# Kernel tuning notes

Hardware: AMD Instinct MI355X
Metric: run time of the kernel (lower is better)

## Reference

```python
import jax, jax.numpy as jnp
import numpy as np

N_NODES = 100000
N_EDGES = 1600000
D_IN = 64
D_HID = 64
NEG_SLOPE = 0.01  # torch leaky_relu default


def _sage_conv(x, src, dst, W_l, b_l, W_r):
    # PyG SAGEConv (mean aggr): lin_l(mean_j x_j) + lin_r(x_i)
    n = x.shape[0]
    msg = x[src]  # [E, D] irregular gather
    agg = jax.ops.segment_sum(msg, dst, num_segments=n)
    deg = jax.ops.segment_sum(jnp.ones((src.shape[0],), x.dtype), dst, num_segments=n)
    mean = agg / jnp.maximum(deg, 1.0)[:, None]
    return mean @ W_l.T + b_l + x @ W_r.T


def setup_inputs() -> dict:
    key = jax.random.key(0)
    ks = jax.random.split(key, 12)
    x = jax.random.normal(ks[0], (N_NODES, D_IN), dtype=jnp.float32)
    edge_index = jax.random.randint(ks[1], (2, N_EDGES), 0, N_NODES, dtype=jnp.int64)
    s = 1.0 / np.sqrt(D_IN)
    params = {}
    dims = [(D_IN, D_HID), (D_HID, D_HID), (D_HID, D_HID)]
    ki = 2
    for i, (din, dout) in enumerate(dims, start=1):
        sc = 1.0 / np.sqrt(din)
        params[f'W_l{i}'] = jax.random.uniform(ks[ki], (dout, din), minval=-sc, maxval=sc, dtype=jnp.float32); ki += 1
        params[f'b_l{i}'] = jnp.zeros((dout,), jnp.float32)
        params[f'W_r{i}'] = jax.random.uniform(ks[ki], (dout, din), minval=-sc, maxval=sc, dtype=jnp.float32); ki += 1
    sc = 1.0 / np.sqrt(D_HID)
    params['W_out'] = jax.random.uniform(ks[ki], (1, D_HID), minval=-sc, maxval=sc, dtype=jnp.float32)
    params['b_out'] = jnp.zeros((1,), jnp.float32)
    return {'x': x, 'edge_index': edge_index, **params}


def reference(x, edge_index, W_l1, b_l1, W_r1, W_l2, b_l2, W_r2, W_l3, b_l3, W_r3, W_out, b_out):
    src, dst = edge_index[0], edge_index[1]
    h = x
    for (Wl, bl, Wr) in ((W_l1, b_l1, W_r1), (W_l2, b_l2, W_r2), (W_l3, b_l3, W_r3)):
        h = _sage_conv(h, src, dst, Wl, bl, Wr)
        h = jnp.where(h >= 0, h, NEG_SLOPE * h)
        # dropout is identity in eval mode
    return h @ W_out.T + b_out  # [N, 1]
```

## Files before the change

kernel.cpp:

```cpp
#include <hip/hip_runtime.h>
#include <hip/hip_fp16.h>

#define D 64
#define NEG_SLOPE 0.01f
#define CB_SHIFT 9
#define CB_NODES 512
#define MAXCB 256
#define CHUNK 4096
#define BCAP 10240
#define SADJ_CAP 10240
#define CGRID 256

typedef _Float16 f16x8 __attribute__((ext_vector_type(8)));
typedef float    f32x4 __attribute__((ext_vector_type(4)));

struct ScatSmem {
    int hist[MAXCB];
    int lofs[MAXCB];
    int gbase[MAXCB];
    int cur[MAXCB];
    int swsum[4];
    unsigned spk[CHUNK];
    unsigned char sbk[CHUNK];
};

__device__ __forceinline__ int detect64(const void* __restrict__ ei) {
    int lane = threadIdx.x & 63;
    int v = ((const int*)ei)[2 * lane + 1];
    return (__ballot(v != 0) == 0ULL) ? 1 : 0;
}

__device__ __forceinline__ int edge_at(const void* __restrict__ ei, long long idx, int is64) {
    if (is64) return (int)((const long long*)ei)[idx];
    return ((const int*)ei)[idx];
}

__device__ __forceinline__ void scatter_body(ScatSmem& sm,
        const void* __restrict__ ei, long long E,
        int* __restrict__ bcursor, unsigned* __restrict__ ebuf,
        int ncb, int bid) {
    int t = threadIdx.x;
    sm.hist[t] = 0;
    int is64 = detect64(ei);
    __syncthreads();
    long long start = (long long)bid * CHUNK;
    int ccnt = (int)min((long long)CHUNK, E - start);

    for (int i = t; i < ccnt; i += 256) {
        int d = edge_at(ei, E + start + i, is64);
        atomicAdd(&sm.hist[d >> CB_SHIFT], 1);
    }
    __syncthreads();
    {
        int v = sm.hist[t];
        int lane = t & 63, w = t >> 6;
        int inc = v;
        for (int off = 1; off < 64; off <<= 1) {
            int u = __shfl_up(inc, off, 64);
            if (lane >= off) inc += u;
        }
        if (lane == 63) sm.swsum[w] = inc;
        __syncthreads();
        int wof = 0;
        for (int i = 0; i < w; ++i) wof += sm.swsum[i];
        sm.lofs[t] = wof + inc - v;
    }
    if (t < ncb && sm.hist[t]) sm.gbase[t] = atomicAdd(&bcursor[t], sm.hist[t]);
    __syncthreads();
    sm.cur[t] = sm.lofs[t];
    __syncthreads();

    for (int i = t; i < ccnt; i += 256) {
        int s = edge_at(ei, start + i, is64);
        int d = edge_at(ei, E + start + i, is64);
        int b = d >> CB_SHIFT;
        int slot = atomicAdd(&sm.cur[b], 1);
        sm.spk[slot] = ((unsigned)s << CB_SHIFT) | (unsigned)(d & (CB_NODES - 1));
        sm.sbk[slot] = (unsigned char)b;
    }
    __syncthreads();

    for (int i = t; i < ccnt; i += 256) {
        int b = sm.sbk[i];
        int dst = sm.gbase[b] + (i - sm.lofs[b]);
        if (dst < BCAP) ebuf[(size_t)b * BCAP + dst] = sm.spk[i];
    }
}

__device__ __forceinline__ void conv_body(const float* __restrict__ x,
        _Float16* __restrict__ x16, long long U, int cid,
        const float* __restrict__ Wl1, const float* __restrict__ Wr1,
        const float* __restrict__ Wl2, const float* __restrict__ Wr2,
        const float* __restrict__ Wl3, const float* __restrict__ Wr3,
        _Float16* __restrict__ W16) {
    int t = threadIdx.x;
    for (long long u = (long long)cid * 256 + t; u < U; u += (long long)CGRID * 256) {
        const float* s = x + u * 8;
        const float4 v0 = *(const float4*)s;
        const float4 v1 = *(const float4*)(s + 4);
        f16x8 o = { (_Float16)v0.x, (_Float16)v0.y, (_Float16)v0.z, (_Float16)v0.w,
                    (_Float16)v1.x, (_Float16)v1.y, (_Float16)v1.z, (_Float16)v1.w };
        *(f16x8*)(x16 + u * 8) = o;
    }
    if (cid == 0) {
        const float* Ws[6] = { Wl1, Wr1, Wl2, Wr2, Wl3, Wr3 };
#pragma unroll
        for (int m = 0; m < 6; ++m) {
            const float* src = Ws[m];
            _Float16* dst = W16 + m * 4096;
            for (int i = t; i < 4096; i += 256) dst[i] = (_Float16)src[i];
        }
    }
}

__global__ __launch_bounds__(256, 6) void scatter_conv_kernel(
        const void* __restrict__ ei, long long E,
        int* __restrict__ bcursor, unsigned* __restrict__ ebuf, int ncb, int sgrid,
        const float* __restrict__ x, _Float16* __restrict__ x16, long long U,
        const float* __restrict__ Wl1, const float* __restrict__ Wr1,
        const float* __restrict__ Wl2, const float* __restrict__ Wr2,
        const float* __restrict__ Wl3, const float* __restrict__ Wr3,
        _Float16* __restrict__ W16) {
    __shared__ ScatSmem sm;
    if ((int)blockIdx.x < sgrid)
        scatter_body(sm, ei, E, bcursor, ebuf, ncb, blockIdx.x);
    else
        conv_body(x, x16, U, blockIdx.x - sgrid, Wl1, Wr1, Wl2, Wr2, Wl3, Wr3, W16);
}

__global__ __launch_bounds__(256) void sage_gemm_kernel(
        const _Float16* __restrict__ Hin, const _Float16* __restrict__ MH,
        const _Float16* __restrict__ W16,
        const float* __restrict__ bl,
        _Float16* __restrict__ Hout,
        const float* __restrict__ Wout, const float* __restrict__ bout,
        float* __restrict__ out, int N, int final_flag) {
    int t = threadIdx.x, w = t >> 6, lane = t & 63;
    int lr = lane & 15;
    int lk = lane >> 4;
    int rbase = (int)blockIdx.x * 128 + w * 32;

    f16x8 ah[2][2], am[2][2];
#pragma unroll
    for (int mt = 0; mt < 2; ++mt) {
        int gn = rbase + mt * 16 + lr;
        if (gn >= N) gn = N - 1;
        const _Float16* hp = Hin + (size_t)gn * D + lk * 8;
        const _Float16* mp = MH  + (size_t)gn * D + lk * 8;
        ah[mt][0] = *(const f16x8*)hp;  ah[mt][1] = *(const f16x8*)(hp + 32);
        am[mt][0] = *(const f16x8*)mp;  am[mt][1] = *(const f16x8*)(mp + 32);
    }

    f32x4 acc[2][4];
#pragma unroll
    for (int mt = 0; mt < 2; ++mt)
#pragma unroll
        for (int nt = 0; nt < 4; ++nt)
            acc[mt][nt] = (f32x4){0.f, 0.f, 0.f, 0.f};

    const _Float16* Wl = W16;
    const _Float16* Wr = W16 + 4096;
#pragma unroll
    for (int nt = 0; nt < 4; ++nt) {
        const _Float16* pl = Wl + (nt * 16 + lr) * D + lk * 8;
        const _Float16* pr = Wr + (nt * 16 + lr) * D + lk * 8;
        f16x8 b0 = *(const f16x8*)pl;  f16x8 b1 = *(const f16x8*)(pl + 32);
        f16x8 c0 = *(const f16x8*)pr;  f16x8 c1 = *(const f16x8*)(pr + 32);
        acc[0][nt] = __builtin_amdgcn_mfma_f32_16x16x32_f16(am[0][0], b0, acc[0][nt], 0, 0, 0);
        acc[0][nt] = __builtin_amdgcn_mfma_f32_16x16x32_f16(am[0][1], b1, acc[0][nt], 0, 0, 0);
        acc[0][nt] = __builtin_amdgcn_mfma_f32_16x16x32_f16(ah[0][0], c0, acc[0][nt], 0, 0, 0);
        acc[0][nt] = __builtin_amdgcn_mfma_f32_16x16x32_f16(ah[0][1], c1, acc[0][nt], 0, 0, 0);
        acc[1][nt] = __builtin_amdgcn_mfma_f32_16x16x32_f16(am[1][0], b0, acc[1][nt], 0, 0, 0);
        acc[1][nt] = __builtin_amdgcn_mfma_f32_16x16x32_f16(am[1][1], b1, acc[1][nt], 0, 0, 0);
        acc[1][nt] = __builtin_amdgcn_mfma_f32_16x16x32_f16(ah[1][0], c0, acc[1][nt], 0, 0, 0);
        acc[1][nt] = __builtin_amdgcn_mfma_f32_16x16x32_f16(ah[1][1], c1, acc[1][nt], 0, 0, 0);
    }

    float blv[4];
#pragma unroll
    for (int nt = 0; nt < 4; ++nt) blv[nt] = bl[nt * 16 + lr];

    if (!final_flag) {
#pragma unroll
        for (int mt = 0; mt < 2; ++mt)
#pragma unroll
            for (int r = 0; r < 4; ++r) {
                int gn = rbase + mt * 16 + lk * 4 + r;
                if (gn < N) {
#pragma unroll
                    for (int nt = 0; nt < 4; ++nt) {
                        float y = acc[mt][nt][r] + blv[nt];
                        y = (y >= 0.f) ? y : NEG_SLOPE * y;
                        Hout[(size_t)gn * D + nt * 16 + lr] = (_Float16)y;
                    }
                }
            }
    } else {
        float wv[4];
#pragma unroll
        for (int nt = 0; nt < 4; ++nt) wv[nt] = Wout[nt * 16 + lr];
        float bo = bout[0];
#pragma unroll
        for (int mt = 0; mt < 2; ++mt)
#pragma unroll
            for (int r = 0; r < 4; ++r) {
                float p = 0.f;
#pragma unroll
                for (int nt = 0; nt < 4; ++nt) {
                    float y = acc[mt][nt][r] + blv[nt];
                    y = (y >= 0.f) ? y : NEG_SLOPE * y;
                    p += y * wv[nt];
                }
                p += __shfl_xor(p, 1, 64);
                p += __shfl_xor(p, 2, 64);
                p += __shfl_xor(p, 4, 64);
                p += __shfl_xor(p, 8, 64);
                int gn = rbase + mt * 16 + lk * 4 + r;
                if (lr == 0 && gn < N) out[gn] = p + bo;
            }
    }
}

__global__ __launch_bounds__(256) void finefill_kernel(
        const unsigned* __restrict__ ebuf, const int* __restrict__ bcount,
        int* __restrict__ rowptr, int* __restrict__ adj, int N, int ncb) {
    __shared__ int cnt[CB_NODES];
    __shared__ int cur[CB_NODES];
    __shared__ int wpart[4];
    __shared__ int wsum4[4];
    __shared__ int se0;
    __shared__ int sAdj[SADJ_CAP];
    int t = threadIdx.x;
    int b = blockIdx.x;

    {
        int v = (t < ncb) ? min(bcount[t], BCAP) : 0;
        int lane = t & 63, w = t >> 6;
        int inc = v;
        for (int off = 1; off < 64; off <<= 1) {
            int u = __shfl_up(inc, off, 64);
            if (lane >= off) inc += u;
        }
        if (lane == 63) wsum4[w] = inc;
        __syncthreads();
        int wof = 0;
        for (int iw = 0; iw < w; ++iw) wof += wsum4[iw];
        int ex = wof + inc - v;
        if (t == b) se0 = ex;
        if (b == 0 && t == 0)
            rowptr[N] = wsum4[0] + wsum4[1] + wsum4[2] + wsum4[3];
    }
    __syncthreads();
    int e0 = se0;
    int len = min(bcount[b], BCAP);
    int nb = b << CB_SHIFT;
    const unsigned* slab = ebuf + (size_t)b * BCAP;

    cnt[2 * t] = 0; cnt[2 * t + 1] = 0;
    __syncthreads();
    for (int i = t; i < len; i += 256) {
        unsigned p = slab[i];
        atomicAdd(&cnt[p & (CB_NODES - 1)], 1);
    }
    __syncthreads();

    int c0 = cnt[2 * t], c1 = cnt[2 * t + 1];
    int s = c0 + c1;
    int lane = t & 63, wv = t >> 6;
    int inc = s;
    for (int off = 1; off < 64; off <<= 1) {
        int u = __shfl_up(inc, off, 64);
        if (lane >= off) inc += u;
    }
    if (lane == 63) wpart[wv] = inc;
    __syncthreads();
    int wof = 0;
    for (int w = 0; w < wv; ++w) wof += wpart[w];
    int ex = wof + inc - s;
    cur[2 * t] = ex; cur[2 * t + 1] = ex + c0;
    {
        int g = nb + 2 * t;
        if (g < N)     rowptr[g]     = e0 + ex;
        if (g + 1 < N) rowptr[g + 1] = e0 + ex + c0;
    }
    __syncthreads();

    int big = (len > SADJ_CAP);
    for (int i = t; i < len; i += 256) {
        unsigned p = slab[i];
        int dl = (int)(p & (CB_NODES - 1));
        int src = (int)(p >> CB_SHIFT);
        int pos = atomicAdd(&cur[dl], 1);
        if (big) adj[e0 + pos] = src;
        else     sAdj[pos] = src;
    }
    __syncthreads();
    if (!big) {
        for (int i = t; i < len; i += 256) adj[e0 + i] = sAdj[i];
    }
}

__global__ __launch_bounds__(256) void agg_kernel(
        const _Float16* __restrict__ H,
        const int* __restrict__ rowptr, const int* __restrict__ adj,
        _Float16* __restrict__ MH, int N) {
    int tid = blockIdx.x * blockDim.x + threadIdx.x;
    int i = tid >> 3;
    int sub = tid & 7;
    if (i >= N) return;

    int b0 = rowptr[i], b1 = rowptr[i + 1];
    float a0 = 0.f, a1 = 0.f, a2 = 0.f, a3 = 0.f;
    float a4 = 0.f, a5 = 0.f, a6 = 0.f, a7 = 0.f;
    size_t cofs = (size_t)(sub << 3);

    int e = b0;
    int nfull = (b1 - b0) >> 2;
#pragma unroll 2
    for (int q = 0; q < nfull; ++q) {
        int s0 = adj[e], s1 = adj[e + 1], s2 = adj[e + 2], s3 = adj[e + 3];
        e += 4;
        union { float4 f4; __half2 h2[4]; } u0, u1, u2, u3;
        u0.f4 = *(const float4*)(H + (size_t)s0 * D + cofs);
        u1.f4 = *(const float4*)(H + (size_t)s1 * D + cofs);
        u2.f4 = *(const float4*)(H + (size_t)s2 * D + cofs);
        u3.f4 = *(const float4*)(H + (size_t)s3 * D + cofs);
#define ACC8(u) { \
        float2 v0 = __half22float2(u.h2[0]); float2 v1 = __half22float2(u.h2[1]); \
        float2 v2 = __half22float2(u.h2[2]); float2 v3 = __half22float2(u.h2[3]); \
        a0 += v0.x; a1 += v0.y; a2 += v1.x; a3 += v1.y; \
        a4 += v2.x; a5 += v2.y; a6 += v3.x; a7 += v3.y; }
        ACC8(u0) ACC8(u1) ACC8(u2) ACC8(u3)
    }
    for (; e < b1; ++e) {
        int s = adj[e];
        union { float4 f4; __half2 h2[4]; } u;
        u.f4 = *(const float4*)(H + (size_t)s * D + cofs);
        ACC8(u)
    }
#undef ACC8

    float inv = 1.0f / fmaxf((float)(b1 - b0), 1.0f);
    f16x8 o = { (_Float16)(a0 * inv), (_Float16)(a1 * inv),
                (_Float16)(a2 * inv), (_Float16)(a3 * inv),
                (_Float16)(a4 * inv), (_Float16)(a5 * inv),
                (_Float16)(a6 * inv), (_Float16)(a7 * inv) };
    *(f16x8*)(MH + (size_t)i * D + cofs) = o;
}

extern "C" void kernel_launch(void* const* d_in, const int* in_sizes, int n_in,
                              void* d_out, int out_size, void* d_ws, size_t ws_size,
                              hipStream_t stream) {
    const float* x    = (const float*)d_in[0];
    const void*  ei   = d_in[1];
    const float* Wl1  = (const float*)d_in[2];
    const float* bl1  = (const float*)d_in[3];
    const float* Wr1  = (const float*)d_in[4];
    const float* Wl2  = (const float*)d_in[5];
    const float* bl2  = (const float*)d_in[6];
    const float* Wr2  = (const float*)d_in[7];
    const float* Wl3  = (const float*)d_in[8];
    const float* bl3  = (const float*)d_in[9];
    const float* Wr3  = (const float*)d_in[10];
    const float* Wout = (const float*)d_in[11];
    const float* bout = (const float*)d_in[12];
    float* out = (float*)d_out;

    int       N = in_sizes[0] / D;
    long long E = (long long)in_sizes[1] / 2;
    int ncb = (N + CB_NODES - 1) >> CB_SHIFT;
    long long U = (long long)N * D / 8;

    char* ws = (char*)d_ws;
    size_t off = 256;
    int* bcursor = (int*)(ws + off); off += 1024;
    int* rowptr = (int*)(ws + off); off += (((size_t)(N + 1) * 4 + 255) / 256) * 256;
    int* adj    = (int*)(ws + off); off += (((size_t)E * 4 + 255) / 256) * 256;
    unsigned* ebuf = (unsigned*)(ws + off); off += (size_t)ncb * BCAP * 4;
    _Float16* x16 = (_Float16*)(ws + off); off += (size_t)N * D * 2;
    _Float16* mh  = (_Float16*)(ws + off); off += (size_t)N * D * 2;
    _Float16* hA  = (_Float16*)(ws + off); off += (size_t)N * D * 2;
    _Float16* hB  = (_Float16*)(ws + off); off += (size_t)N * D * 2;
    _Float16* W16 = (_Float16*)(ws + off); off += 6 * 4096 * 2;

    int sgrid = (int)((E + CHUNK - 1) / CHUNK);
    int ggrid = (N + 127) / 128;
    int agrid = (N * 8 + 255) / 256;

    hipMemsetAsync(bcursor, 0, 1024, stream);

    scatter_conv_kernel<<<sgrid + CGRID, 256, 0, stream>>>(
        ei, E, bcursor, ebuf, ncb, sgrid,
        x, x16, U, Wl1, Wr1, Wl2, Wr2, Wl3, Wr3, W16);
    finefill_kernel<<<ncb, 256, 0, stream>>>(ebuf, bcursor, rowptr, adj, N, ncb);
    agg_kernel<<<agrid, 256, 0, stream>>>(x16, rowptr, adj, mh, N);
    sage_gemm_kernel<<<ggrid, 256, 0, stream>>>(x16, mh, W16, bl1, hA,
                                                Wout, bout, out, N, 0);
    agg_kernel<<<agrid, 256, 0, stream>>>(hA, rowptr, adj, mh, N);
    sage_gemm_kernel<<<ggrid, 256, 0, stream>>>(hA, mh, W16 + 2 * 4096, bl2, hB,
                                                Wout, bout, out, N, 0);
    agg_kernel<<<agrid, 256, 0, stream>>>(hB, rowptr, adj, mh, N);
    sage_gemm_kernel<<<ggrid, 256, 0, stream>>>(hB, mh, W16 + 4 * 4096, bl3, hA,
                                                Wout, bout, out, N, 1);
}
```

Before: 272.8 us.

## Fuse neighbor mean aggregation into SAGE GEMM kernel via shared memory

Each layer's aggregation kernel and GEMM kernel are merged into one kernel. Every block first gathers and averages neighbor features for its 128 nodes into padded shared memory, then runs the MFMA GEMM reading the mean from LDS. This removes the global round trip of the mean buffer and three kernel launches. In exchange, the gather now runs with fewer threads per node-group: 100k nodes over 782 blocks, with each thread looping over 4 nodes serially. That may reduce memory-level parallelism for the irregular gather.

```diff
diff --git a/kernel.cpp b/kernel.cpp
--- a/kernel.cpp
+++ b/kernel.cpp
@@ -10,6 +10,7 @@
 #define BCAP 10240
 #define SADJ_CAP 10240
 #define CGRID 256
+#define SAH 72
 
 typedef _Float16 f16x8 __attribute__((ext_vector_type(8)));
 typedef float    f32x4 __attribute__((ext_vector_type(4)));
@@ -128,17 +129,70 @@
         conv_body(x, x16, U, blockIdx.x - sgrid, Wl1, Wr1, Wl2, Wr2, Wl3, Wr3, W16);
 }
 
-__global__ __launch_bounds__(256) void sage_gemm_kernel(
-        const _Float16* __restrict__ Hin, const _Float16* __restrict__ MH,
+__global__ __launch_bounds__(256) void agg_gemm_kernel(
+        const _Float16* __restrict__ Hin,
+        const int* __restrict__ rowptr, const int* __restrict__ adj,
         const _Float16* __restrict__ W16,
         const float* __restrict__ bl,
         _Float16* __restrict__ Hout,
         const float* __restrict__ Wout, const float* __restrict__ bout,
         float* __restrict__ out, int N, int final_flag) {
-    int t = threadIdx.x, w = t >> 6, lane = t & 63;
+    __shared__ _Float16 smh[128 * SAH];
+    int t = threadIdx.x;
+    int node_base = (int)blockIdx.x * 128;
+
+    {
+        int g = t >> 3;
+        int sub = t & 7;
+        size_t cofs = (size_t)(sub << 3);
+#pragma unroll
+        for (int p = 0; p < 4; ++p) {
+            int local = p * 32 + g;
+            int i = node_base + local;
+            float a0 = 0.f, a1 = 0.f, a2 = 0.f, a3 = 0.f;
+            float a4 = 0.f, a5 = 0.f, a6 = 0.f, a7 = 0.f;
+            float inv = 0.f;
+            if (i < N) {
+                int b0 = rowptr[i], b1 = rowptr[i + 1];
+                int e = b0;
+                int nfull = (b1 - b0) >> 2;
+                for (int q = 0; q < nfull; ++q) {
+                    int s0 = adj[e], s1 = adj[e + 1], s2 = adj[e + 2], s3 = adj[e + 3];
+                    e += 4;
+                    union { float4 f4; __half2 h2[4]; } u0, u1, u2, u3;
+                    u0.f4 = *(const float4*)(Hin + (size_t)s0 * D + cofs);
+                    u1.f4 = *(const float4*)(Hin + (size_t)s1 * D + cofs);
+                    u2.f4 = *(const float4*)(Hin + (size_t)s2 * D + cofs);
+                    u3.f4 = *(const float4*)(Hin + (size_t)s3 * D + cofs);
+#define ACC8(u) { \
+        float2 v0 = __half22float2(u.h2[0]); float2 v1 = __half22float2(u.h2[1]); \
+        float2 v2 = __half22float2(u.h2[2]); float2 v3 = __half22float2(u.h2[3]); \
+        a0 += v0.x; a1 += v0.y; a2 += v1.x; a3 += v1.y; \
+        a4 += v2.x; a5 += v2.y; a6 += v3.x; a7 += v3.y; }
+                    ACC8(u0) ACC8(u1) ACC8(u2) ACC8(u3)
+                }
+                for (; e < b1; ++e) {
+                    int s = adj[e];
+                    union { float4 f4; __half2 h2[4]; } u;
+                    u.f4 = *(const float4*)(Hin + (size_t)s * D + cofs);
+                    ACC8(u)
+                }
+#undef ACC8
+                inv = 1.0f / fmaxf((float)(b1 - b0), 1.0f);
+            }
+            f16x8 o = { (_Float16)(a0 * inv), (_Float16)(a1 * inv),
+                        (_Float16)(a2 * inv), (_Float16)(a3 * inv),
+                        (_Float16)(a4 * inv), (_Float16)(a5 * inv),
+                        (_Float16)(a6 * inv), (_Float16)(a7 * inv) };
+            *(f16x8*)(smh + local * SAH + (sub << 3)) = o;
+        }
+    }
+    __syncthreads();
+
+    int w = t >> 6, lane = t & 63;
     int lr = lane & 15;
     int lk = lane >> 4;
-    int rbase = (int)blockIdx.x * 128 + w * 32;
+    int rbase = node_base + w * 32;
 
     f16x8 ah[2][2], am[2][2];
 #pragma unroll
@@ -146,8 +200,8 @@
         int gn = rbase + mt * 16 + lr;
         if (gn >= N) gn = N - 1;
         const _Float16* hp = Hin + (size_t)gn * D + lk * 8;
-        const _Float16* mp = MH  + (size_t)gn * D + lk * 8;
         ah[mt][0] = *(const f16x8*)hp;  ah[mt][1] = *(const f16x8*)(hp + 32);
+        const _Float16* mp = smh + (w * 32 + mt * 16 + lr) * SAH + lk * 8;
         am[mt][0] = *(const f16x8*)mp;  am[mt][1] = *(const f16x8*)(mp + 32);
     }
 
@@ -298,54 +352,6 @@
     if (!big) {
         for (int i = t; i < len; i += 256) adj[e0 + i] = sAdj[i];
     }
-}
-
-__global__ __launch_bounds__(256) void agg_kernel(
-        const _Float16* __restrict__ H,
-        const int* __restrict__ rowptr, const int* __restrict__ adj,
-        _Float16* __restrict__ MH, int N) {
-    int tid = blockIdx.x * blockDim.x + threadIdx.x;
-    int i = tid >> 3;
-    int sub = tid & 7;
-    if (i >= N) return;
-
-    int b0 = rowptr[i], b1 = rowptr[i + 1];
-    float a0 = 0.f, a1 = 0.f, a2 = 0.f, a3 = 0.f;
-    float a4 = 0.f, a5 = 0.f, a6 = 0.f, a7 = 0.f;
-    size_t cofs = (size_t)(sub << 3);
-
-    int e = b0;
-    int nfull = (b1 - b0) >> 2;
-#pragma unroll 2
-    for (int q = 0; q < nfull; ++q) {
-        int s0 = adj[e], s1 = adj[e + 1], s2 = adj[e + 2], s3 = adj[e + 3];
-        e += 4;
-        union { float4 f4; __half2 h2[4]; } u0, u1, u2, u3;
-        u0.f4 = *(const float4*)(H + (size_t)s0 * D + cofs);
-        u1.f4 = *(const float4*)(H + (size_t)s1 * D + cofs);
-        u2.f4 = *(const float4*)(H + (size_t)s2 * D + cofs);
-        u3.f4 = *(const float4*)(H + (size_t)s3 * D + cofs);
-#define ACC8(u) { \
-        float2 v0 = __half22float2(u.h2[0]); float2 v1 = __half22float2(u.h2[1]); \
-        float2 v2 = __half22float2(u.h2[2]); float2 v3 = __half22float2(u.h2[3]); \
-        a0 += v0.x; a1 += v0.y; a2 += v1.x; a3 += v1.y; \
-        a4 += v2.x; a5 += v2.y; a6 += v3.x; a7 += v3.y; }
-        ACC8(u0) ACC8(u1) ACC8(u2) ACC8(u3)
-    }
-    for (; e < b1; ++e) {
-        int s = adj[e];
-        union { float4 f4; __half2 h2[4]; } u;
-        u.f4 = *(const float4*)(H + (size_t)s * D + cofs);
-        ACC8(u)
-    }
-#undef ACC8
-
-    float inv = 1.0f / fmaxf((float)(b1 - b0), 1.0f);
-    f16x8 o = { (_Float16)(a0 * inv), (_Float16)(a1 * inv),
-                (_Float16)(a2 * inv), (_Float16)(a3 * inv),
-                (_Float16)(a4 * inv), (_Float16)(a5 * inv),
-                (_Float16)(a6 * inv), (_Float16)(a7 * inv) };
-    *(f16x8*)(MH + (size_t)i * D + cofs) = o;
 }
 
 extern "C" void kernel_launch(void* const* d_in, const int* in_sizes, int n_in,
@@ -378,14 +384,12 @@
     int* adj    = (int*)(ws + off); off += (((size_t)E * 4 + 255) / 256) * 256;
     unsigned* ebuf = (unsigned*)(ws + off); off += (size_t)ncb * BCAP * 4;
     _Float16* x16 = (_Float16*)(ws + off); off += (size_t)N * D * 2;
-    _Float16* mh  = (_Float16*)(ws + off); off += (size_t)N * D * 2;
     _Float16* hA  = (_Float16*)(ws + off); off += (size_t)N * D * 2;
     _Float16* hB  = (_Float16*)(ws + off); off += (size_t)N * D * 2;
     _Float16* W16 = (_Float16*)(ws + off); off += 6 * 4096 * 2;
 
     int sgrid = (int)((E + CHUNK - 1) / CHUNK);
     int ggrid = (N + 127) / 128;
-    int agrid = (N * 8 + 255) / 256;
 
     hipMemsetAsync(bcursor, 0, 1024, stream);
 
@@ -393,13 +397,10 @@
         ei, E, bcursor, ebuf, ncb, sgrid,
         x, x16, U, Wl1, Wr1, Wl2, Wr2, Wl3, Wr3, W16);
     finefill_kernel<<<ncb, 256, 0, stream>>>(ebuf, bcursor, rowptr, adj, N, ncb);
-    agg_kernel<<<agrid, 256, 0, stream>>>(x16, rowptr, adj, mh, N);
-    sage_gemm_kernel<<<ggrid, 256, 0, stream>>>(x16, mh, W16, bl1, hA,
-                                                Wout, bout, out, N, 0);
-    agg_kernel<<<agrid, 256, 0, stream>>>(hA, rowptr, adj, mh, N);
-    sage_gemm_kernel<<<ggrid, 256, 0, stream>>>(hA, mh, W16 + 2 * 4096, bl2, hB,
-                                                Wout, bout, out, N, 0);
-    agg_kernel<<<agrid, 256, 0, stream>>>(hB, rowptr, adj, mh, N);
-    sage_gemm_kernel<<<ggrid, 256, 0, stream>>>(hB, mh, W16 + 4 * 4096, bl3, hA,
-                                                Wout, bout, out, N, 1);
-}
+    agg_gemm_kernel<<<ggrid, 256, 0, stream>>>(x16, rowptr, adj, W16, bl1, hA,
+                                               Wout, bout, out, N, 0);
+    agg_gemm_kernel<<<ggrid, 256, 0, stream>>>(hA, rowptr, adj, W16 + 2 * 4096, bl2, hB,
+                                               Wout, bout, out, N, 0);
+    agg_gemm_kernel<<<ggrid, 256, 0, stream>>>(hB, rowptr, adj, W16 + 4 * 4096, bl3, hA,
+                                               Wout, bout, out, N, 1);
+}
```

New measurement: 261.8 us. 1.04x faster.
